# Performance work log

Hardware: AMD Instinct MI355X
Metric: run time of the kernel (lower is better)

## Reference

```python
import jax, jax.numpy as jnp
import numpy as np

HIDDEN_DIM = 2048
N = 4  # expansion_rate
LAYER_IDX = 0
S_ALPHA = 0.01
S_BETA = 0.01
EPS = 1e-5


def setup_inputs() -> dict:
    key = jax.random.key(0)
    k1, k2, k3, k4, k5 = jax.random.split(key, 5)
    batch, seq = 4, 2048
    layer_output = jax.random.normal(k1, (batch, seq, HIDDEN_DIM), dtype=jnp.float32)
    hidden_states = jax.random.normal(k2, (batch, seq, N, HIDDEN_DIM), dtype=jnp.float32)
    # static base matrices (initialization from the torch module)
    B = jnp.ones((1, N), dtype=jnp.float32)
    Am = jnp.zeros((N, 1), dtype=jnp.float32).at[LAYER_IDX % N, 0].set(1.0)
    Ar = jnp.eye(N, dtype=jnp.float32)
    # dynamic parameters
    s_alpha = jnp.full((N, N), S_ALPHA, dtype=jnp.float32)
    s_beta = jnp.full((1, N), S_BETA, dtype=jnp.float32)
    W_beta = jax.random.normal(k3, (HIDDEN_DIM, N), dtype=jnp.float32) * 0.02
    W_m = jax.random.normal(k4, (HIDDEN_DIM, N), dtype=jnp.float32) * 0.02
    W_r = jax.random.normal(k5, (HIDDEN_DIM, N, N), dtype=jnp.float32) * 0.02
    return {
        "layer_output": layer_output,
        "hidden_states": hidden_states,
        "B": B,
        "Am": Am,
        "Ar": Ar,
        "s_alpha": s_alpha,
        "s_beta": s_beta,
        "W_beta": W_beta,
        "W_m": W_m,
        "W_r": W_r,
    }


def reference(layer_output, hidden_states, B, Am, Ar, s_alpha, s_beta, W_beta, W_m, W_r):
    # hidden_states: [b, s, n, d]; layer_output: [b, s, d]
    # --- dynamic matrices ---
    mu = jnp.mean(hidden_states, axis=-1, keepdims=True)
    var = jnp.var(hidden_states, axis=-1, keepdims=True)
    H_norm = (hidden_states - mu) * jax.lax.rsqrt(var + EPS)  # layer_norm, no affine
    H_bar = H_norm.mean(axis=2)  # [b, s, d]

    delta_B = jnp.tanh(H_bar @ W_beta)            # [b, s, n]
    B_dyn = s_beta[0] * delta_B + B[0]            # [b, s, n]
    delta_Am = jnp.tanh(H_bar @ W_m)              # [b, s, n]
    Am_dyn = s_alpha[:, 0] * delta_Am + Am[:, 0]  # [b, s, n]
    delta_Ar = jnp.tanh(jnp.einsum('bsd,dij->bsij', H_bar, W_r))  # [b, s, n, n]
    Ar_dyn = s_alpha * delta_Ar + Ar              # [b, s, n, n]

    # --- combine ---
    depth = B_dyn[..., None] * layer_output[:, :, None, :]                       # [b,s,n,d]
    mixed = jnp.einsum('bsn,bsnd->bsd', Am_dyn, hidden_states)[:, :, None, :]    # [b,s,1,d] broadcasts over n
    residual = jnp.einsum('bsij,bsjd->bsid', Ar_dyn, hidden_states)              # [b,s,n,d]
    return depth + mixed + residual
```

## Files before the change

### kernel.cpp

```cpp
#include <hip/hip_runtime.h>
#include <hip/hip_fp16.h>

#define D     2048
#define BLK   512
#define EPSV  1e-5f

typedef _Float16 h2 __attribute__((ext_vector_type(2)));

__device__ __forceinline__ unsigned int pkh(float a, float b) {
    return __builtin_bit_cast(unsigned int, __builtin_amdgcn_cvt_pkrtz(a, b));
}
__device__ __forceinline__ h2 ash2(unsigned int u) {
    return __builtin_bit_cast(h2, u);
}

template<int CTRL>
__device__ __forceinline__ float dppadd(float x) {
    int y = __builtin_amdgcn_update_dpp(0, __builtin_bit_cast(int, x), CTRL, 0xf, 0xf, false);
    return x + __builtin_bit_cast(float, y);
}
__device__ __forceinline__ float wave_sum(float x) {
    x += __shfl_xor(x, 32, 64);
    x += __shfl_xor(x, 16, 64);
    x = dppadd<0x111>(x);
    x = dppadd<0x112>(x);
    x = dppadd<0x114>(x);
    x = dppadd<0x118>(x);
    return x;
}

__device__ __forceinline__ float rdlane(float v, int l) {
    return __builtin_bit_cast(float, __builtin_amdgcn_readlane(__builtin_bit_cast(int, v), l));
}

__global__ __launch_bounds__(256) void wt_kernel(
    const float* __restrict__ Wb, const float* __restrict__ Wm,
    const float* __restrict__ Wr, unsigned int* __restrict__ Wq,
    float* __restrict__ S)
{
    const int c = blockIdx.x;
    const int t = threadIdx.x;
    const float* src;
    int stride;
    if (c < 4)       { src = Wb + c;       stride = 4;  }
    else if (c < 8)  { src = Wm + (c - 4); stride = 4;  }
    else             { src = Wr + (c - 8); stride = 16; }

    float s = 0.f;
    #pragma unroll
    for (int k = 0; k < 4; ++k) {
        int p = t + 256 * k;
        float a = src[(2 * p)     * stride];
        float b = src[(2 * p + 1) * stride];
        s += a + b;
        Wq[c * 1024 + p] = pkh(a, b);
    }
    __shared__ float rsum[4];
    #pragma unroll
    for (int off = 32; off; off >>= 1) s += __shfl_xor(s, off, 64);
    if ((t & 63) == 0) rsum[t >> 6] = s;
    __syncthreads();
    if (t == 0) S[c] = rsum[0] + rsum[1] + rsum[2] + rsum[3];
}

__global__ __launch_bounds__(BLK) void hc_kernel(
    const float* __restrict__ lo,
    const float* __restrict__ hs,
    const float* __restrict__ Bm,
    const float* __restrict__ Am,
    const float* __restrict__ Ar,
    const float* __restrict__ s_alpha,
    const float* __restrict__ s_beta,
    const unsigned int* __restrict__ Wq,
    const float* __restrict__ S,
    float* __restrict__ out)
{
    __shared__ __align__(16) unsigned int hq[4][1024];
    __shared__ float Rl[24][4];
    __shared__ float sred[8][2];

    const int tid  = threadIdx.x;
    const int wave = tid >> 6;
    const int lane = tid & 63;
    const int row  = wave >> 1;
    const int half = wave & 1;
    const long tok = blockIdx.x;

    const float4* hs4  = (const float4*)(hs + tok * (long)(4 * D));
    const float4* lo4  = (const float4*)(lo + tok * (long)D);
    float4*       out4 = (float4*)(out + tok * (long)(4 * D));

    float4 hv[4];
    const int base = row * 512 + half * 256 + lane;
    #pragma unroll
    for (int k = 0; k < 4; ++k) hv[k] = hs4[base + 64 * k];
    float4 lv = lo4[tid];

    float s = 0.f, q = 0.f;
    uint2* hq2w = (uint2*)hq[row];
    #pragma unroll
    for (int k = 0; k < 4; ++k) {
        float4 v = hv[k];
        s += v.x + v.y + v.z + v.w;
        q += v.x * v.x + v.y * v.y + v.z * v.z + v.w * v.w;
        uint2 p;
        p.x = pkh(v.x, v.y);
        p.y = pkh(v.z, v.w);
        hq2w[half * 256 + 64 * k + lane] = p;
    }
    s = wave_sum(s);
    q = wave_sum(q);
    if (lane == 15) { sred[wave][0] = s; sred[wave][1] = q; }
    __syncthreads();

    float acc[3][4];
    #pragma unroll
    for (int j = 0; j < 3; ++j)
        #pragma unroll
        for (int n = 0; n < 4; ++n) acc[j][n] = 0.f;

    const int c0 = wave * 3;
    const uint2* Wq2 = (const uint2*)Wq;

    #pragma unroll
    for (int k = 0; k < 8; ++k) {
        int i = 64 * k + lane;
        uint2 hr[4];
        #pragma unroll
        for (int n = 0; n < 4; ++n) hr[n] = ((const uint2*)hq[n])[i];
        uint2 wv[3];
        #pragma unroll
        for (int j = 0; j < 3; ++j) wv[j] = Wq2[(c0 + j) * 512 + i];
        #pragma unroll
        for (int j = 0; j < 3; ++j)
            #pragma unroll
            for (int n = 0; n < 4; ++n) {
                acc[j][n] = __builtin_amdgcn_fdot2(ash2(hr[n].x), ash2(wv[j].x), acc[j][n], false);
                acc[j][n] = __builtin_amdgcn_fdot2(ash2(hr[n].y), ash2(wv[j].y), acc[j][n], false);
            }
    }
    #pragma unroll
    for (int j = 0; j < 3; ++j)
        #pragma unroll
        for (int n = 0; n < 4; ++n) {
            float v = wave_sum(acc[j][n]);
            if (lane == 15) Rl[c0 + j][n] = v;
        }
    __syncthreads();

    float cv = 0.f;
    if (lane < 24) {
        int c = lane;
        float Sc = S[c];
        float raw = 0.f;
        #pragma unroll
        for (int n = 0; n < 4; ++n) {
            float ss = sred[2 * n][0] + sred[2 * n + 1][0];
            float qq = sred[2 * n][1] + sred[2 * n + 1][1];
            float m   = ss * (1.f / D);
            float var = qq * (1.f / D) - m * m;
            float r   = rsqrtf(var + EPSV);
            raw += r * (Rl[c][n] - m * Sc);
        }
        raw *= 0.25f;
        float t = tanhf(raw);
        if (c < 4) {
            cv = s_beta[c] * t + Bm[c];
        } else if (c < 8) {
            int n = c - 4;
            cv = s_alpha[n * 4] * t + Am[n];
        } else {
            int ij = c - 8;
            cv = s_alpha[ij] * t + Ar[ij];
        }
    }
    float Bd[4], Amd[4], Ard[4][4];
    #pragma unroll
    for (int n = 0; n < 4; ++n) {
        Bd[n]  = rdlane(cv, n);
        Amd[n] = rdlane(cv, 4 + n);
    }
    #pragma unroll
    for (int i = 0; i < 4; ++i)
        #pragma unroll
        for (int j = 0; j < 4; ++j) Ard[i][j] = rdlane(cv, 8 + i * 4 + j);

    float4 h[4];
    #pragma unroll
    for (int n = 0; n < 4; ++n) {
        uint2 r = ((const uint2*)hq[n])[tid];
        h2 a = ash2(r.x), b = ash2(r.y);
        h[n].x = (float)a[0]; h[n].y = (float)a[1];
        h[n].z = (float)b[0]; h[n].w = (float)b[1];
    }
    float4 mx = {0.f, 0.f, 0.f, 0.f};
    #pragma unroll
    for (int n = 0; n < 4; ++n) {
        mx.x += Amd[n] * h[n].x; mx.y += Amd[n] * h[n].y;
        mx.z += Amd[n] * h[n].z; mx.w += Amd[n] * h[n].w;
    }
    #pragma unroll
    for (int i = 0; i < 4; ++i) {
        float4 o;
        o.x = Bd[i] * lv.x + mx.x;
        o.y = Bd[i] * lv.y + mx.y;
        o.z = Bd[i] * lv.z + mx.z;
        o.w = Bd[i] * lv.w + mx.w;
        #pragma unroll
        for (int j = 0; j < 4; ++j) {
            o.x += Ard[i][j] * h[j].x;
            o.y += Ard[i][j] * h[j].y;
            o.z += Ard[i][j] * h[j].z;
            o.w += Ard[i][j] * h[j].w;
        }
        out4[i * 512 + tid] = o;
    }
}

extern "C" void kernel_launch(void* const* d_in, const int* in_sizes, int n_in,
                              void* d_out, int out_size, void* d_ws, size_t ws_size,
                              hipStream_t stream) {
    const float* lo      = (const float*)d_in[0];
    const float* hs      = (const float*)d_in[1];
    const float* Bm      = (const float*)d_in[2];
    const float* Am      = (const float*)d_in[3];
    const float* Ar      = (const float*)d_in[4];
    const float* s_alpha = (const float*)d_in[5];
    const float* s_beta  = (const float*)d_in[6];
    const float* Wb      = (const float*)d_in[7];
    const float* Wm      = (const float*)d_in[8];
    const float* Wr      = (const float*)d_in[9];
    float* out = (float*)d_out;

    unsigned int* Wq = (unsigned int*)d_ws;
    float* S         = (float*)((char*)d_ws + 24 * 1024 * 4);

    wt_kernel<<<24, 256, 0, stream>>>(Wb, Wm, Wr, Wq, S);

    const int tokens = in_sizes[0] / D;
    hc_kernel<<<tokens, BLK, 0, stream>>>(lo, hs, Bm, Am, Ar, s_alpha, s_beta,
                                          Wq, S, out);
}
```

Before: 143.3 us.

## Compute per-token projection with bf16 MFMA instead of fp16 dot2 loops

```diff
diff --git a/kernel.cpp b/kernel.cpp
--- a/kernel.cpp
+++ b/kernel.cpp
@@ -1,17 +1,22 @@
 #include <hip/hip_runtime.h>
-#include <hip/hip_fp16.h>
 
 #define D     2048
 #define BLK   512
 #define EPSV  1e-5f
 
-typedef _Float16 h2 __attribute__((ext_vector_type(2)));
-
-__device__ __forceinline__ unsigned int pkh(float a, float b) {
-    return __builtin_bit_cast(unsigned int, __builtin_amdgcn_cvt_pkrtz(a, b));
-}
-__device__ __forceinline__ h2 ash2(unsigned int u) {
-    return __builtin_bit_cast(h2, u);
+typedef short  s16x8 __attribute__((ext_vector_type(8)));
+typedef float  f32x4 __attribute__((ext_vector_type(4)));
+
+__device__ __forceinline__ unsigned int pk2(float x, float y) {
+    unsigned int r;
+    asm volatile("v_cvt_pk_bf16_f32 %0, %1, %2" : "=v"(r) : "v"(x), "v"(y));
+    return r;
+}
+__device__ __forceinline__ float bl(unsigned int u) {
+    union { unsigned int x; float f; } v; v.x = u << 16; return v.f;
+}
+__device__ __forceinline__ float bh(unsigned int u) {
+    union { unsigned int x; float f; } v; v.x = u & 0xffff0000u; return v.f;
 }
 
 template<int CTRL>
@@ -53,7 +58,7 @@
         float a = src[(2 * p)     * stride];
         float b = src[(2 * p + 1) * stride];
         s += a + b;
-        Wq[c * 1024 + p] = pkh(a, b);
+        Wq[c * 1024 + p] = pk2(a, b);
     }
     __shared__ float rsum[4];
     #pragma unroll
@@ -75,8 +80,8 @@
     const float* __restrict__ S,
     float* __restrict__ out)
 {
-    __shared__ __align__(16) unsigned int hq[4][1024];
-    __shared__ float Rl[24][4];
+    __shared__ __align__(16) unsigned int hq[4][1028];
+    __shared__ float pred[8][24][4];
     __shared__ float sred[8][2];
 
     const int tid  = threadIdx.x;
@@ -104,8 +109,8 @@
         s += v.x + v.y + v.z + v.w;
         q += v.x * v.x + v.y * v.y + v.z * v.z + v.w * v.w;
         uint2 p;
-        p.x = pkh(v.x, v.y);
-        p.y = pkh(v.z, v.w);
+        p.x = pk2(v.x, v.y);
+        p.y = pk2(v.z, v.w);
         hq2w[half * 256 + 64 * k + lane] = p;
     }
     s = wave_sum(s);
@@ -113,39 +118,32 @@
     if (lane == 15) { sred[wave][0] = s; sred[wave][1] = q; }
     __syncthreads();
 
-    float acc[3][4];
-    #pragma unroll
-    for (int j = 0; j < 3; ++j)
-        #pragma unroll
-        for (int n = 0; n < 4; ++n) acc[j][n] = 0.f;
-
-    const int c0 = wave * 3;
-    const uint2* Wq2 = (const uint2*)Wq;
-
-    #pragma unroll
-    for (int k = 0; k < 8; ++k) {
-        int i = 64 * k + lane;
-        uint2 hr[4];
-        #pragma unroll
-        for (int n = 0; n < 4; ++n) hr[n] = ((const uint2*)hq[n])[i];
-        uint2 wv[3];
-        #pragma unroll
-        for (int j = 0; j < 3; ++j) wv[j] = Wq2[(c0 + j) * 512 + i];
-        #pragma unroll
-        for (int j = 0; j < 3; ++j)
-            #pragma unroll
-            for (int n = 0; n < 4; ++n) {
-                acc[j][n] = __builtin_amdgcn_fdot2(ash2(hr[n].x), ash2(wv[j].x), acc[j][n], false);
-                acc[j][n] = __builtin_amdgcn_fdot2(ash2(hr[n].y), ash2(wv[j].y), acc[j][n], false);
-            }
-    }
-    #pragma unroll
-    for (int j = 0; j < 3; ++j)
-        #pragma unroll
-        for (int n = 0; n < 4; ++n) {
-            float v = wave_sum(acc[j][n]);
-            if (lane == 15) Rl[c0 + j][n] = v;
-        }
+    f32x4 acc0 = {0.f, 0.f, 0.f, 0.f};
+    f32x4 acc1 = {0.f, 0.f, 0.f, 0.f};
+    const int kg    = lane >> 4;
+    const int arow  = lane & 3;
+    const int bcol0 = lane & 15;
+    const int bcol1 = 16 + (lane & 7);
+    const uint4* hqA = (const uint4*)hq[arow];
+    const uint4* Wq4 = (const uint4*)Wq;
+
+    #pragma unroll
+    for (int st = 0; st < 8; ++st) {
+        int idx = (wave * 8 + st) * 4 + kg;
+        s16x8 a  = __builtin_bit_cast(s16x8, hqA[idx]);
+        s16x8 b0 = __builtin_bit_cast(s16x8, Wq4[bcol0 * 256 + idx]);
+        s16x8 b1 = __builtin_bit_cast(s16x8, Wq4[bcol1 * 256 + idx]);
+        acc0 = __builtin_amdgcn_mfma_f32_16x16x32_bf16(a, b0, acc0, 0, 0, 0);
+        acc1 = __builtin_amdgcn_mfma_f32_16x16x32_bf16(a, b1, acc1, 0, 0, 0);
+    }
+    if (lane < 16) {
+        #pragma unroll
+        for (int r = 0; r < 4; ++r) pred[wave][lane][r] = acc0[r];
+    }
+    if (lane < 8) {
+        #pragma unroll
+        for (int r = 0; r < 4; ++r) pred[wave][16 + lane][r] = acc1[r];
+    }
     __syncthreads();
 
     float cv = 0.f;
@@ -155,12 +153,15 @@
         float raw = 0.f;
         #pragma unroll
         for (int n = 0; n < 4; ++n) {
+            float R = 0.f;
+            #pragma unroll
+            for (int w = 0; w < 8; ++w) R += pred[w][c][n];
             float ss = sred[2 * n][0] + sred[2 * n + 1][0];
             float qq = sred[2 * n][1] + sred[2 * n + 1][1];
             float m   = ss * (1.f / D);
             float var = qq * (1.f / D) - m * m;
             float r   = rsqrtf(var + EPSV);
-            raw += r * (Rl[c][n] - m * Sc);
+            raw += r * (R - m * Sc);
         }
         raw *= 0.25f;
         float t = tanhf(raw);
@@ -189,9 +190,8 @@
     #pragma unroll
     for (int n = 0; n < 4; ++n) {
         uint2 r = ((const uint2*)hq[n])[tid];
-        h2 a = ash2(r.x), b = ash2(r.y);
-        h[n].x = (float)a[0]; h[n].y = (float)a[1];
-        h[n].z = (float)b[0]; h[n].w = (float)b[1];
+        h[n].x = bl(r.x); h[n].y = bh(r.x);
+        h[n].z = bl(r.y); h[n].w = bh(r.y);
     }
     float4 mx = {0.f, 0.f, 0.f, 0.f};
     #pragma unroll
```

Result: slower. 196.0 us (+36.8%).

## Map one token per wave and compute normalized mean before projection

Applied to the files above, without the earlier changes.

```diff
diff --git a/kernel.cpp b/kernel.cpp
--- a/kernel.cpp
+++ b/kernel.cpp
@@ -2,7 +2,6 @@
 #include <hip/hip_fp16.h>
 
 #define D     2048
-#define BLK   512
 #define EPSV  1e-5f
 
 typedef _Float16 h2 __attribute__((ext_vector_type(2)));
@@ -33,10 +32,15 @@
     return __builtin_bit_cast(float, __builtin_amdgcn_readlane(__builtin_bit_cast(int, v), l));
 }
 
+__device__ __forceinline__ float ftanh(float x) {
+    float xc = fminf(fmaxf(x, -10.f), 10.f);
+    float e  = __expf(2.f * xc);
+    return 1.f - 2.f * __builtin_amdgcn_rcpf(e + 1.f);
+}
+
 __global__ __launch_bounds__(256) void wt_kernel(
     const float* __restrict__ Wb, const float* __restrict__ Wm,
-    const float* __restrict__ Wr, unsigned int* __restrict__ Wq,
-    float* __restrict__ S)
+    const float* __restrict__ Wr, unsigned int* __restrict__ Wq)
 {
     const int c = blockIdx.x;
     const int t = threadIdx.x;
@@ -46,24 +50,16 @@
     else if (c < 8)  { src = Wm + (c - 4); stride = 4;  }
     else             { src = Wr + (c - 8); stride = 16; }
 
-    float s = 0.f;
     #pragma unroll
     for (int k = 0; k < 4; ++k) {
         int p = t + 256 * k;
         float a = src[(2 * p)     * stride];
         float b = src[(2 * p + 1) * stride];
-        s += a + b;
         Wq[c * 1024 + p] = pkh(a, b);
     }
-    __shared__ float rsum[4];
-    #pragma unroll
-    for (int off = 32; off; off >>= 1) s += __shfl_xor(s, off, 64);
-    if ((t & 63) == 0) rsum[t >> 6] = s;
-    __syncthreads();
-    if (t == 0) S[c] = rsum[0] + rsum[1] + rsum[2] + rsum[3];
-}
-
-__global__ __launch_bounds__(BLK) void hc_kernel(
+}
+
+__global__ __launch_bounds__(256) void hc_kernel(
     const float* __restrict__ lo,
     const float* __restrict__ hs,
     const float* __restrict__ Bm,
@@ -72,148 +68,110 @@
     const float* __restrict__ s_alpha,
     const float* __restrict__ s_beta,
     const unsigned int* __restrict__ Wq,
-    const float* __restrict__ S,
     float* __restrict__ out)
 {
-    __shared__ __align__(16) unsigned int hq[4][1024];
-    __shared__ float Rl[24][4];
-    __shared__ float sred[8][2];
-
     const int tid  = threadIdx.x;
     const int wave = tid >> 6;
     const int lane = tid & 63;
-    const int row  = wave >> 1;
-    const int half = wave & 1;
-    const long tok = blockIdx.x;
+    const long tok = (long)blockIdx.x * 4 + wave;
 
     const float4* hs4  = (const float4*)(hs + tok * (long)(4 * D));
     const float4* lo4  = (const float4*)(lo + tok * (long)D);
     float4*       out4 = (float4*)(out + tok * (long)(4 * D));
 
-    float4 hv[4];
-    const int base = row * 512 + half * 256 + lane;
-    #pragma unroll
-    for (int k = 0; k < 4; ++k) hv[k] = hs4[base + 64 * k];
-    float4 lv = lo4[tid];
-
-    float s = 0.f, q = 0.f;
-    uint2* hq2w = (uint2*)hq[row];
-    #pragma unroll
-    for (int k = 0; k < 4; ++k) {
-        float4 v = hv[k];
-        s += v.x + v.y + v.z + v.w;
-        q += v.x * v.x + v.y * v.y + v.z * v.z + v.w * v.w;
-        uint2 p;
-        p.x = pkh(v.x, v.y);
-        p.y = pkh(v.z, v.w);
-        hq2w[half * 256 + 64 * k + lane] = p;
-    }
-    s = wave_sum(s);
-    q = wave_sum(q);
-    if (lane == 15) { sred[wave][0] = s; sred[wave][1] = q; }
-    __syncthreads();
-
-    float acc[3][4];
-    #pragma unroll
-    for (int j = 0; j < 3; ++j)
+    float mu[4], rs[4];
+    #pragma unroll
+    for (int n = 0; n < 4; ++n) {
+        float s = 0.f, q = 0.f;
         #pragma unroll
-        for (int n = 0; n < 4; ++n) acc[j][n] = 0.f;
-
-    const int c0 = wave * 3;
+        for (int k = 0; k < 8; ++k) {
+            float4 v = hs4[n * 512 + k * 64 + lane];
+            s += v.x + v.y + v.z + v.w;
+            q += v.x * v.x + v.y * v.y + v.z * v.z + v.w * v.w;
+        }
+        s = wave_sum(s);
+        q = wave_sum(q);
+        float st = rdlane(s, 15), qt = rdlane(q, 15);
+        float m  = st * (1.f / D);
+        mu[n] = m;
+        rs[n] = rsqrtf(qt * (1.f / D) - m * m + EPSV);
+    }
+
+    float acc[24];
+    #pragma unroll
+    for (int c = 0; c < 24; ++c) acc[c] = 0.f;
+
     const uint2* Wq2 = (const uint2*)Wq;
 
     #pragma unroll
     for (int k = 0; k < 8; ++k) {
-        int i = 64 * k + lane;
-        uint2 hr[4];
+        int i4 = k * 64 + lane;
+        float4 v0 = hs4[0 * 512 + i4];
+        float4 v1 = hs4[1 * 512 + i4];
+        float4 v2 = hs4[2 * 512 + i4];
+        float4 v3 = hs4[3 * 512 + i4];
+        float hbx = 0.25f * ((v0.x - mu[0]) * rs[0] + (v1.x - mu[1]) * rs[1] +
+                             (v2.x - mu[2]) * rs[2] + (v3.x - mu[3]) * rs[3]);
+        float hby = 0.25f * ((v0.y - mu[0]) * rs[0] + (v1.y - mu[1]) * rs[1] +
+                             (v2.y - mu[2]) * rs[2] + (v3.y - mu[3]) * rs[3]);
+        float hbz = 0.25f * ((v0.z - mu[0]) * rs[0] + (v1.z - mu[1]) * rs[1] +
+                             (v2.z - mu[2]) * rs[2] + (v3.z - mu[3]) * rs[3]);
+        float hbw = 0.25f * ((v0.w - mu[0]) * rs[0] + (v1.w - mu[1]) * rs[1] +
+                             (v2.w - mu[2]) * rs[2] + (v3.w - mu[3]) * rs[3]);
+        h2 plo = ash2(pkh(hbx, hby));
+        h2 phi = ash2(pkh(hbz, hbw));
         #pragma unroll
-        for (int n = 0; n < 4; ++n) hr[n] = ((const uint2*)hq[n])[i];
-        uint2 wv[3];
+        for (int c = 0; c < 24; ++c) {
+            uint2 w = Wq2[c * 512 + i4];
+            acc[c] = __builtin_amdgcn_fdot2(plo, ash2(w.x), acc[c], false);
+            acc[c] = __builtin_amdgcn_fdot2(phi, ash2(w.y), acc[c], false);
+        }
+    }
+
+    #pragma unroll
+    for (int c = 0; c < 24; ++c) acc[c] = wave_sum(acc[c]);
+
+    float coef[24];
+    #pragma unroll
+    for (int c = 0; c < 24; ++c) {
+        float R = rdlane(acc[c], 15);
+        float t = ftanh(R);
+        float cv;
+        if (c < 4)      cv = s_beta[c] * t + Bm[c];
+        else if (c < 8) cv = s_alpha[(c - 4) * 4] * t + Am[c - 4];
+        else            cv = s_alpha[c - 8] * t + Ar[c - 8];
+        coef[c] = cv;
+    }
+
+    #pragma unroll
+    for (int k = 0; k < 8; ++k) {
+        int i4 = k * 64 + lane;
+        float4 v0 = hs4[0 * 512 + i4];
+        float4 v1 = hs4[1 * 512 + i4];
+        float4 v2 = hs4[2 * 512 + i4];
+        float4 v3 = hs4[3 * 512 + i4];
+        float4 lv = lo4[i4];
+
+        float4 mx;
+        mx.x = coef[4] * v0.x + coef[5] * v1.x + coef[6] * v2.x + coef[7] * v3.x;
+        mx.y = coef[4] * v0.y + coef[5] * v1.y + coef[6] * v2.y + coef[7] * v3.y;
+        mx.z = coef[4] * v0.z + coef[5] * v1.z + coef[6] * v2.z + coef[7] * v3.z;
+        mx.w = coef[4] * v0.w + coef[5] * v1.w + coef[6] * v2.w + coef[7] * v3.w;
+
         #pragma unroll
-        for (int j = 0; j < 3; ++j) wv[j] = Wq2[(c0 + j) * 512 + i];
-        #pragma unroll
-        for (int j = 0; j < 3; ++j)
-            #pragma unroll
-            for (int n = 0; n < 4; ++n) {
-                acc[j][n] = __builtin_amdgcn_fdot2(ash2(hr[n].x), ash2(wv[j].x), acc[j][n], false);
-                acc[j][n] = __builtin_amdgcn_fdot2(ash2(hr[n].y), ash2(wv[j].y), acc[j][n], false);
-            }
-    }
-    #pragma unroll
-    for (int j = 0; j < 3; ++j)
-        #pragma unroll
-        for (int n = 0; n < 4; ++n) {
-            float v = wave_sum(acc[j][n]);
-            if (lane == 15) Rl[c0 + j][n] = v;
+        for (int i = 0; i < 4; ++i) {
+            float a0 = coef[8 + i * 4 + 0];
+            float a1 = coef[8 + i * 4 + 1];
+            float a2 = coef[8 + i * 4 + 2];
+            float a3 = coef[8 + i * 4 + 3];
+            float bd = coef[i];
+            float4 o;
+            o.x = bd * lv.x + mx.x + a0 * v0.x + a1 * v1.x + a2 * v2.x + a3 * v3.x;
+            o.y = bd * lv.y + mx.y + a0 * v0.y + a1 * v1.y + a2 * v2.y + a3 * v3.y;
+            o.z = bd * lv.z + mx.z + a0 * v0.z + a1 * v1.z + a2 * v2.z + a3 * v3.z;
+            o.w = bd * lv.w + mx.w + a0 * v0.w + a1 * v1.w + a2 * v2.w + a3 * v3.w;
+            out4[i * 512 + i4] = o;
         }
-    __syncthreads();
-
-    float cv = 0.f;
-    if (lane < 24) {
-        int c = lane;
-        float Sc = S[c];
-        float raw = 0.f;
-        #pragma unroll
-        for (int n = 0; n < 4; ++n) {
-            float ss = sred[2 * n][0] + sred[2 * n + 1][0];
-            float qq = sred[2 * n][1] + sred[2 * n + 1][1];
-            float m   = ss * (1.f / D);
-            float var = qq * (1.f / D) - m * m;
-            float r   = rsqrtf(var + EPSV);
-            raw += r * (Rl[c][n] - m * Sc);
-        }
-        raw *= 0.25f;
-        float t = tanhf(raw);
-        if (c < 4) {
-            cv = s_beta[c] * t + Bm[c];
-        } else if (c < 8) {
-            int n = c - 4;
-            cv = s_alpha[n * 4] * t + Am[n];
-        } else {
-            int ij = c - 8;
-            cv = s_alpha[ij] * t + Ar[ij];
-        }
-    }
-    float Bd[4], Amd[4], Ard[4][4];
-    #pragma unroll
-    for (int n = 0; n < 4; ++n) {
-        Bd[n]  = rdlane(cv, n);
-        Amd[n] = rdlane(cv, 4 + n);
-    }
-    #pragma unroll
-    for (int i = 0; i < 4; ++i)
-        #pragma unroll
-        for (int j = 0; j < 4; ++j) Ard[i][j] = rdlane(cv, 8 + i * 4 + j);
-
-    float4 h[4];
-    #pragma unroll
-    for (int n = 0; n < 4; ++n) {
-        uint2 r = ((const uint2*)hq[n])[tid];
-        h2 a = ash2(r.x), b = ash2(r.y);
-        h[n].x = (float)a[0]; h[n].y = (float)a[1];
-        h[n].z = (float)b[0]; h[n].w = (float)b[1];
-    }
-    float4 mx = {0.f, 0.f, 0.f, 0.f};
-    #pragma unroll
-    for (int n = 0; n < 4; ++n) {
-        mx.x += Amd[n] * h[n].x; mx.y += Amd[n] * h[n].y;
-        mx.z += Amd[n] * h[n].z; mx.w += Amd[n] * h[n].w;
-    }
-    #pragma unroll
-    for (int i = 0; i < 4; ++i) {
-        float4 o;
-        o.x = Bd[i] * lv.x + mx.x;
-        o.y = Bd[i] * lv.y + mx.y;
-        o.z = Bd[i] * lv.z + mx.z;
-        o.w = Bd[i] * lv.w + mx.w;
-        #pragma unroll
-        for (int j = 0; j < 4; ++j) {
-            o.x += Ard[i][j] * h[j].x;
-            o.y += Ard[i][j] * h[j].y;
-            o.z += Ard[i][j] * h[j].z;
-            o.w += Ard[i][j] * h[j].w;
-        }
-        out4[i * 512 + tid] = o;
     }
 }
 
@@ -233,11 +191,10 @@
     float* out = (float*)d_out;
 
     unsigned int* Wq = (unsigned int*)d_ws;
-    float* S         = (float*)((char*)d_ws + 24 * 1024 * 4);
-
-    wt_kernel<<<24, 256, 0, stream>>>(Wb, Wm, Wr, Wq, S);
+
+    wt_kernel<<<24, 256, 0, stream>>>(Wb, Wm, Wr, Wq);
 
     const int tokens = in_sizes[0] / D;
-    hc_kernel<<<tokens, BLK, 0, stream>>>(lo, hs, Bm, Am, Ar, s_alpha, s_beta,
-                                          Wq, S, out);
-}
+    hc_kernel<<<tokens / 4, 256, 0, stream>>>(lo, hs, Bm, Am, Ar, s_alpha, s_beta,
+                                              Wq, out);
+}
```

Result: slower. 296.5 us (+106.9%).

## Process 16 tokens per block with double-buffered async LDS prefetch

Applied to the files above, without the earlier changes.

```diff
diff --git a/kernel.cpp b/kernel.cpp
--- a/kernel.cpp
+++ b/kernel.cpp
@@ -3,6 +3,7 @@
 
 #define D     2048
 #define BLK   512
+#define TPB   16
 #define EPSV  1e-5f
 
 typedef _Float16 h2 __attribute__((ext_vector_type(2)));
@@ -31,6 +32,12 @@
 
 __device__ __forceinline__ float rdlane(float v, int l) {
     return __builtin_bit_cast(float, __builtin_amdgcn_readlane(__builtin_bit_cast(int, v), l));
+}
+
+__device__ __forceinline__ void gld16(const float* g, float* l) {
+    __builtin_amdgcn_global_load_lds(
+        (const __attribute__((address_space(1))) unsigned int*)g,
+        (__attribute__((address_space(3))) unsigned int*)l, 16, 0, 0);
 }
 
 __global__ __launch_bounds__(256) void wt_kernel(
@@ -75,145 +82,153 @@
     const float* __restrict__ S,
     float* __restrict__ out)
 {
-    __shared__ __align__(16) unsigned int hq[4][1024];
+    __shared__ __align__(16) float hbuf[2][4][D];
     __shared__ float Rl[24][4];
     __shared__ float sred[8][2];
 
     const int tid  = threadIdx.x;
     const int wave = tid >> 6;
     const int lane = tid & 63;
-    const int row  = wave >> 1;
-    const int half = wave & 1;
-    const long tok = blockIdx.x;
-
-    const float4* hs4  = (const float4*)(hs + tok * (long)(4 * D));
-    const float4* lo4  = (const float4*)(lo + tok * (long)D);
-    float4*       out4 = (float4*)(out + tok * (long)(4 * D));
-
-    float4 hv[4];
-    const int base = row * 512 + half * 256 + lane;
-    #pragma unroll
-    for (int k = 0; k < 4; ++k) hv[k] = hs4[base + 64 * k];
-    float4 lv = lo4[tid];
-
-    float s = 0.f, q = 0.f;
-    uint2* hq2w = (uint2*)hq[row];
-    #pragma unroll
-    for (int k = 0; k < 4; ++k) {
-        float4 v = hv[k];
-        s += v.x + v.y + v.z + v.w;
-        q += v.x * v.x + v.y * v.y + v.z * v.z + v.w * v.w;
-        uint2 p;
-        p.x = pkh(v.x, v.y);
-        p.y = pkh(v.z, v.w);
-        hq2w[half * 256 + 64 * k + lane] = p;
+    const long tok0 = (long)blockIdx.x * TPB;
+    const uint2* Wq2 = (const uint2*)Wq;
+
+    {
+        const float* g = hs + tok0 * (long)(4 * D) + wave * 1024 + lane * 4;
+        float*       l = &hbuf[0][0][0] + wave * 1024;
+        #pragma unroll
+        for (int k = 0; k < 4; ++k) gld16(g + k * 256, l + k * 256);
     }
-    s = wave_sum(s);
-    q = wave_sum(q);
-    if (lane == 15) { sred[wave][0] = s; sred[wave][1] = q; }
+    float4 lva = ((const float4*)(lo + tok0 * (long)D))[tid];
+    float4 lvb;
+    asm volatile("s_waitcnt vmcnt(0)" ::: "memory");
     __syncthreads();
 
-    float acc[3][4];
-    #pragma unroll
-    for (int j = 0; j < 3; ++j)
-        #pragma unroll
-        for (int n = 0; n < 4; ++n) acc[j][n] = 0.f;
-
-    const int c0 = wave * 3;
-    const uint2* Wq2 = (const uint2*)Wq;
-
-    #pragma unroll
-    for (int k = 0; k < 8; ++k) {
-        int i = 64 * k + lane;
-        uint2 hr[4];
-        #pragma unroll
-        for (int n = 0; n < 4; ++n) hr[n] = ((const uint2*)hq[n])[i];
-        uint2 wv[3];
-        #pragma unroll
-        for (int j = 0; j < 3; ++j) wv[j] = Wq2[(c0 + j) * 512 + i];
+    auto step = [&](int buf, float4& lv, float4& lvn, long tok, bool pf) {
+        if (pf) {
+            const float* g = hs + (tok + 1) * (long)(4 * D) + wave * 1024 + lane * 4;
+            float*       l = &hbuf[buf ^ 1][0][0] + wave * 1024;
+            #pragma unroll
+            for (int k = 0; k < 4; ++k) gld16(g + k * 256, l + k * 256);
+            lvn = ((const float4*)(lo + (tok + 1) * (long)D))[tid];
+        }
+
+        {
+            const int row = wave >> 1, half = wave & 1;
+            const float4* hr = (const float4*)&hbuf[buf][row][half * 1024];
+            float s = 0.f, q = 0.f;
+            #pragma unroll
+            for (int k = 0; k < 4; ++k) {
+                float4 v = hr[k * 64 + lane];
+                s += v.x + v.y + v.z + v.w;
+                q += v.x * v.x + v.y * v.y + v.z * v.z + v.w * v.w;
+            }
+            s = wave_sum(s);
+            q = wave_sum(q);
+            if (lane == 15) { sred[wave][0] = s; sred[wave][1] = q; }
+        }
+
+        float acc[3][4];
         #pragma unroll
         for (int j = 0; j < 3; ++j)
             #pragma unroll
+            for (int n = 0; n < 4; ++n) acc[j][n] = 0.f;
+        const int c0 = wave * 3;
+
+        #pragma unroll
+        for (int i = 0; i < 8; ++i) {
+            int i4 = i * 64 + lane;
+            h2 plo[4], phi[4];
+            #pragma unroll
             for (int n = 0; n < 4; ++n) {
-                acc[j][n] = __builtin_amdgcn_fdot2(ash2(hr[n].x), ash2(wv[j].x), acc[j][n], false);
-                acc[j][n] = __builtin_amdgcn_fdot2(ash2(hr[n].y), ash2(wv[j].y), acc[j][n], false);
-            }
-    }
-    #pragma unroll
-    for (int j = 0; j < 3; ++j)
+                float4 v = ((const float4*)hbuf[buf][n])[i4];
+                plo[n] = ash2(pkh(v.x, v.y));
+                phi[n] = ash2(pkh(v.z, v.w));
+            }
+            uint2 wv[3];
+            #pragma unroll
+            for (int j = 0; j < 3; ++j) wv[j] = Wq2[(c0 + j) * 512 + i4];
+            #pragma unroll
+            for (int j = 0; j < 3; ++j)
+                #pragma unroll
+                for (int n = 0; n < 4; ++n) {
+                    acc[j][n] = __builtin_amdgcn_fdot2(plo[n], ash2(wv[j].x), acc[j][n], false);
+                    acc[j][n] = __builtin_amdgcn_fdot2(phi[n], ash2(wv[j].y), acc[j][n], false);
+                }
+        }
+        #pragma unroll
+        for (int j = 0; j < 3; ++j)
+            #pragma unroll
+            for (int n = 0; n < 4; ++n) {
+                float v = wave_sum(acc[j][n]);
+                if (lane == 15) Rl[c0 + j][n] = v;
+            }
+        __syncthreads();
+
+        float cv = 0.f;
+        if (lane < 24) {
+            int c = lane;
+            float Sc = S[c];
+            float raw = 0.f;
+            #pragma unroll
+            for (int n = 0; n < 4; ++n) {
+                float ss = sred[2 * n][0] + sred[2 * n + 1][0];
+                float qq = sred[2 * n][1] + sred[2 * n + 1][1];
+                float m   = ss * (1.f / D);
+                float var = qq * (1.f / D) - m * m;
+                float r   = rsqrtf(var + EPSV);
+                raw += r * (Rl[c][n] - m * Sc);
+            }
+            raw *= 0.25f;
+            float t = tanhf(raw);
+            if (c < 4)      cv = s_beta[c] * t + Bm[c];
+            else if (c < 8) cv = s_alpha[(c - 4) * 4] * t + Am[c - 4];
+            else            cv = s_alpha[c - 8] * t + Ar[c - 8];
+        }
+        float Bd[4], Amd[4], Ard[4][4];
         #pragma unroll
         for (int n = 0; n < 4; ++n) {
-            float v = wave_sum(acc[j][n]);
-            if (lane == 15) Rl[c0 + j][n] = v;
-        }
-    __syncthreads();
-
-    float cv = 0.f;
-    if (lane < 24) {
-        int c = lane;
-        float Sc = S[c];
-        float raw = 0.f;
+            Bd[n]  = rdlane(cv, n);
+            Amd[n] = rdlane(cv, 4 + n);
+        }
+        #pragma unroll
+        for (int i = 0; i < 4; ++i)
+            #pragma unroll
+            for (int j = 0; j < 4; ++j) Ard[i][j] = rdlane(cv, 8 + i * 4 + j);
+
+        float4 h[4];
+        #pragma unroll
+        for (int n = 0; n < 4; ++n) h[n] = ((const float4*)hbuf[buf][n])[tid];
+        float4* out4 = (float4*)(out + tok * (long)(4 * D));
+        float4 mx = {0.f, 0.f, 0.f, 0.f};
         #pragma unroll
         for (int n = 0; n < 4; ++n) {
-            float ss = sred[2 * n][0] + sred[2 * n + 1][0];
-            float qq = sred[2 * n][1] + sred[2 * n + 1][1];
-            float m   = ss * (1.f / D);
-            float var = qq * (1.f / D) - m * m;
-            float r   = rsqrtf(var + EPSV);
-            raw += r * (Rl[c][n] - m * Sc);
-        }
-        raw *= 0.25f;
-        float t = tanhf(raw);
-        if (c < 4) {
-            cv = s_beta[c] * t + Bm[c];
-        } else if (c < 8) {
-            int n = c - 4;
-            cv = s_alpha[n * 4] * t + Am[n];
-        } else {
-            int ij = c - 8;
-            cv = s_alpha[ij] * t + Ar[ij];
-        }
-    }
-    float Bd[4], Amd[4], Ard[4][4];
-    #pragma unroll
-    for (int n = 0; n < 4; ++n) {
-        Bd[n]  = rdlane(cv, n);
-        Amd[n] = rdlane(cv, 4 + n);
-    }
-    #pragma unroll
-    for (int i = 0; i < 4; ++i)
-        #pragma unroll
-        for (int j = 0; j < 4; ++j) Ard[i][j] = rdlane(cv, 8 + i * 4 + j);
-
-    float4 h[4];
-    #pragma unroll
-    for (int n = 0; n < 4; ++n) {
-        uint2 r = ((const uint2*)hq[n])[tid];
-        h2 a = ash2(r.x), b = ash2(r.y);
-        h[n].x = (float)a[0]; h[n].y = (float)a[1];
-        h[n].z = (float)b[0]; h[n].w = (float)b[1];
-    }
-    float4 mx = {0.f, 0.f, 0.f, 0.f};
-    #pragma unroll
-    for (int n = 0; n < 4; ++n) {
-        mx.x += Amd[n] * h[n].x; mx.y += Amd[n] * h[n].y;
-        mx.z += Amd[n] * h[n].z; mx.w += Amd[n] * h[n].w;
-    }
-    #pragma unroll
-    for (int i = 0; i < 4; ++i) {
-        float4 o;
-        o.x = Bd[i] * lv.x + mx.x;
-        o.y = Bd[i] * lv.y + mx.y;
-        o.z = Bd[i] * lv.z + mx.z;
-        o.w = Bd[i] * lv.w + mx.w;
-        #pragma unroll
-        for (int j = 0; j < 4; ++j) {
-            o.x += Ard[i][j] * h[j].x;
-            o.y += Ard[i][j] * h[j].y;
-            o.z += Ard[i][j] * h[j].z;
-            o.w += Ard[i][j] * h[j].w;
-        }
-        out4[i * 512 + tid] = o;
+            mx.x += Amd[n] * h[n].x; mx.y += Amd[n] * h[n].y;
+            mx.z += Amd[n] * h[n].z; mx.w += Amd[n] * h[n].w;
+        }
+        #pragma unroll
+        for (int i = 0; i < 4; ++i) {
+            float4 o;
+            o.x = Bd[i] * lv.x + mx.x;
+            o.y = Bd[i] * lv.y + mx.y;
+            o.z = Bd[i] * lv.z + mx.z;
+            o.w = Bd[i] * lv.w + mx.w;
+            #pragma unroll
+            for (int j = 0; j < 4; ++j) {
+                o.x += Ard[i][j] * h[j].x;
+                o.y += Ard[i][j] * h[j].y;
+                o.z += Ard[i][j] * h[j].z;
+                o.w += Ard[i][j] * h[j].w;
+            }
+            out4[i * 512 + tid] = o;
+        }
+
+        asm volatile("s_waitcnt vmcnt(0)" ::: "memory");
+        __syncthreads();
+    };
+
+    for (int t = 0; t < TPB; t += 2) {
+        step(0, lva, lvb, tok0 + t,     true);
+        step(1, lvb, lva, tok0 + t + 1, t + 2 < TPB);
     }
 }
 
@@ -238,6 +253,6 @@
     wt_kernel<<<24, 256, 0, stream>>>(Wb, Wm, Wr, Wq, S);
 
     const int tokens = in_sizes[0] / D;
-    hc_kernel<<<tokens, BLK, 0, stream>>>(lo, hs, Bm, Am, Ar, s_alpha, s_beta,
-                                          Wq, S, out);
-}
+    hc_kernel<<<tokens / TPB, BLK, 0, stream>>>(lo, hs, Bm, Am, Ar, s_alpha, s_beta,
+                                                Wq, S, out);
+}
```

After: 304.6 us. +112.5%, slower.
